# Performance work log

Hardware: AMD Instinct MI355X
Metric: run time of the kernel (lower is better)

Reference implementation:

```python
import jax, jax.numpy as jnp
import numpy as np

EMB = 128
HID = 128
N = 1024


def setup_inputs() -> dict:
    key = jax.random.key(0)
    ks = jax.random.split(key, 10)
    s1 = 1.0 / np.sqrt(2 * EMB)
    s2 = 1.0 / np.sqrt(HID)
    return {
        "z1": jax.random.normal(ks[0], (N, EMB), jnp.float32),
        "z2": jax.random.normal(ks[1], (N, EMB), jnp.float32),
        "W1": jax.random.uniform(ks[2], (HID, 2 * EMB), jnp.float32, -s1, s1),
        "b1": jax.random.uniform(ks[3], (HID,), jnp.float32, -s1, s1),
        "W2": jax.random.uniform(ks[4], (HID, HID), jnp.float32, -s2, s2),
        "b2": jax.random.uniform(ks[5], (HID,), jnp.float32, -s2, s2),
        "W3": jax.random.uniform(ks[6], (1, HID), jnp.float32, -s2, s2),
        "b3": jax.random.uniform(ks[7], (1,), jnp.float32, -s2, s2),
    }


def reference(z1, z2, W1, b1, W2, b2, W3, b3):
    # pairs[i, j] = concat(z1[j], z2[i]); first Linear split into two matmuls
    # so the [n, n, 2*emb] concat tensor is never materialized (same math).
    W1a = W1[:, :EMB]   # acts on z1 half
    W1b = W1[:, EMB:]   # acts on z2 half
    a = jnp.einsum('jd,hd->jh', z1, W1a)          # [n, h], varies along j
    b = jnp.einsum('id,hd->ih', z2, W1b)          # [n, h], varies along i
    h1 = jax.nn.gelu(a[None, :, :] + b[:, None, :] + b1, approximate=False)  # [n, n, h]
    h2 = jax.nn.gelu(jnp.einsum('ijh,gh->ijg', h1, W2) + b2, approximate=False)
    log_q = jnp.einsum('ijh,oh->ijo', h2, W3) + b3  # [n, n, 1]
    return log_q[..., 0]
```

## Files before the change

kernel.cpp:

```cpp
#include <hip/hip_runtime.h>

#define NN  1024
#define EMB 128
#define HID 128

typedef __attribute__((ext_vector_type(4))) float float4v;
typedef __attribute__((ext_vector_type(8))) float float8v;
typedef __attribute__((ext_vector_type(8))) short short8;
typedef __attribute__((ext_vector_type(4))) __bf16 bf16x4;
typedef __attribute__((ext_vector_type(8))) __bf16 bf16x8;

__device__ __forceinline__ short8 to_bf16x8(float4v a, float4v b) {
  float8v f = {a[0], a[1], a[2], a[3], b[0], b[1], b[2], b[3]};
  bf16x8 r = __builtin_convertvector(f, bf16x8);
  return __builtin_bit_cast(short8, r);
}

__device__ __forceinline__ void store_bf16x4(short* p, float4v v) {
  bf16x4 r = __builtin_convertvector(v, bf16x4);
  *(bf16x4*)p = r;
}

__device__ __forceinline__ float4v gelu4(float4v x) {
  float4v x2 = x * x;
  float4v t = x2 * 0.1029432f + 2.3022086f;
  float4v y = x * t;
  float4v e;
  e[0] = __builtin_amdgcn_exp2f(y[0]);
  e[1] = __builtin_amdgcn_exp2f(y[1]);
  e[2] = __builtin_amdgcn_exp2f(y[2]);
  e[3] = __builtin_amdgcn_exp2f(y[3]);
  float4v d = e + 1.0f;
  float p01 = d[0] * d[1];
  float p23 = d[2] * d[3];
  float rall = __builtin_amdgcn_rcpf(p01 * p23);
  float r01 = p23 * rall;
  float r23 = p01 * rall;
  float4v rv;
  rv[0] = d[1] * r01;
  rv[1] = d[0] * r01;
  rv[2] = d[3] * r23;
  rv[3] = d[2] * r23;
  return x - x * rv;
}

__device__ __forceinline__ float4v mfma16(short8 a, short8 b, float4v c) {
  return __builtin_amdgcn_mfma_f32_16x16x32_bf16(a, b, c, 0, 0, 0);
}

__global__ __launch_bounds__(256)
void prep_kernel(const float* __restrict__ z1, const float* __restrict__ z2,
                 const float* __restrict__ W1, const float* __restrict__ b1,
                 const float* __restrict__ W2,
                 float* __restrict__ Abuf, float* __restrict__ Bbuf,
                 unsigned short* __restrict__ W2f) {
  int blk = blockIdx.x, tid = threadIdx.x;
  if (blk < 128) {
    int which = blk >> 6;
    int j0 = (blk & 63) << 4;
    const float* z = which ? z2 : z1;
    __shared__ __align__(16) short zf[4 * 64 * 8];
    __shared__ __align__(16) short w1f[HID * HID];

    {
      int row = tid >> 4;
      int col = (tid & 15) * 8;
      const float* zp = z + (j0 + row) * EMB + col;
      float4v v0 = *(const float4v*)zp;
      float4v v1 = *(const float4v*)(zp + 4);
      int kt = col >> 5;
      int lane = ((col >> 3) & 3) * 16 + row;
      *(short8*)(zf + (kt * 64 + lane) * 8) = to_bf16x8(v0, v1);
    }
    {
      const float* wbase = W1 + which * EMB;
#pragma unroll
      for (int p = 0; p < 16; ++p) {
        int u = p * 256 + tid;
        int g = u >> 5;
        int c = (u & 31) * 4;
        float4v v = *(const float4v*)(wbase + g * (2 * EMB) + c);
        int kt = c >> 5;
        int nt = g >> 4;
        int lane = ((c >> 3) & 3) * 16 + (g & 15);
        store_bf16x4(w1f + ((kt * 8 + nt) * 64 + lane) * 8 + (c & 7), v);
      }
    }
    __syncthreads();

    int w = tid >> 6, l = tid & 63, r = l & 15, q = l >> 4;
    float4v acc0 = {}, acc1 = {};
#pragma unroll
    for (int kt = 0; kt < 4; ++kt) {
      short8 az  = *(const short8*)(zf + (kt * 64 + l) * 8);
      short8 bf0 = *(const short8*)(w1f + ((kt * 8 + w * 2) * 64 + l) * 8);
      short8 bf1 = *(const short8*)(w1f + ((kt * 8 + w * 2 + 1) * 64 + l) * 8);
      acc0 = mfma16(az, bf0, acc0);
      acc1 = mfma16(az, bf1, acc1);
    }
    float ba0 = which ? 0.0f : b1[w * 32 + r];
    float ba1 = which ? 0.0f : b1[w * 32 + 16 + r];
    float* dstp = which ? Bbuf : Abuf;
#pragma unroll
    for (int reg = 0; reg < 4; ++reg) {
      int row = j0 + q * 4 + reg;
      dstp[row * HID + w * 32 + r]      = acc0[reg] + ba0;
      dstp[row * HID + w * 32 + 16 + r] = acc1[reg] + ba1;
    }
  } else {
    int idx = (blk - 128) * 2048 + tid * 8;
    int lane = (idx >> 3) & 63;
    int nt = (idx >> 9) & 7;
    int kt = idx >> 12;
    int g = nt * 16 + (lane & 15);
    int hb = kt * 32 + (lane >> 4) * 8;
#pragma unroll
    for (int j = 0; j < 8; ++j) {
      unsigned u = __float_as_uint(W2[g * HID + hb + j]);
      W2f[idx + j] = (unsigned short)((u + 0x7FFFu + ((u >> 16) & 1u)) >> 16);
    }
  }
}

__global__ __launch_bounds__(512, 6)
void fused_mlp_kernel(const float* __restrict__ Abuf, const float* __restrict__ Bbuf,
                      const float* __restrict__ W2f4,
                      const float* __restrict__ b2, const float* __restrict__ W3,
                      const float* __restrict__ b3, float* __restrict__ out) {
  __shared__ __align__(16) short s_w2[HID * HID];

  int tid = threadIdx.x;
  {
    const float4v* src = (const float4v*)W2f4;
    float4v* dst = (float4v*)s_w2;
#pragma unroll
    for (int t = 0; t < 4; ++t)
      dst[tid + t * 512] = src[tid + t * 512];
  }

  int w = tid >> 6, l = tid & 63, r = l & 15, q = l >> 4;
  int bi = (blockIdx.x >> 6) << 3;
  int bj = (blockIdx.x & 63) << 4;

  const float* Arow = Abuf + (bj + r) * HID;
  const float* Brow = Bbuf + (bi + w) * HID;

  float4v acc[8];
#pragma unroll
  for (int nt = 0; nt < 8; ++nt) {
    float bv = b2[nt * 16 + r];
    acc[nt] = (float4v){bv, bv, bv, bv};
  }

  __syncthreads();

#pragma unroll
  for (int kt = 0; kt < 4; ++kt) {
    int h0 = kt * 32 + q * 8;
    float4v a0 = *(const float4v*)(Arow + h0);
    float4v a1 = *(const float4v*)(Arow + h0 + 4);
    float4v c0 = *(const float4v*)(Brow + h0);
    float4v c1 = *(const float4v*)(Brow + h0 + 4);
    short8 af = to_bf16x8(gelu4(a0 + c0), gelu4(a1 + c1));

    const short8* wrow = (const short8*)s_w2 + kt * 8 * 64 + l;
#pragma unroll
    for (int nt = 0; nt < 8; ++nt)
      acc[nt] = mfma16(af, wrow[nt * 64], acc[nt]);
  }

  float4v s = {0.f, 0.f, 0.f, 0.f};
#pragma unroll
  for (int nt = 0; nt < 8; ++nt) {
    float wv = W3[nt * 16 + r];
    s = s + gelu4(acc[nt]) * wv;
  }
#pragma unroll
  for (int mask = 1; mask < 16; mask <<= 1) {
#pragma unroll
    for (int reg = 0; reg < 4; ++reg)
      s[reg] += __shfl_xor(s[reg], mask, 64);
  }
  if (r < 4) {
    int irow = bi + w;
    int jcol = bj + q * 4 + r;
    out[irow * NN + jcol] = s[r] + b3[0];
  }
}

extern "C" void kernel_launch(void* const* d_in, const int* in_sizes, int n_in,
                              void* d_out, int out_size, void* d_ws, size_t ws_size,
                              hipStream_t stream) {
  const float* z1 = (const float*)d_in[0];
  const float* z2 = (const float*)d_in[1];
  const float* W1 = (const float*)d_in[2];
  const float* b1 = (const float*)d_in[3];
  const float* W2 = (const float*)d_in[4];
  const float* b2 = (const float*)d_in[5];
  const float* W3 = (const float*)d_in[6];
  const float* b3 = (const float*)d_in[7];
  float* out = (float*)d_out;

  float* Abuf = (float*)d_ws;
  float* Bbuf = Abuf + NN * HID;
  unsigned short* W2f = (unsigned short*)(Bbuf + NN * HID);

  prep_kernel<<<136, 256, 0, stream>>>(z1, z2, W1, b1, W2, Abuf, Bbuf, W2f);
  fused_mlp_kernel<<<(NN / 8) * (NN / 16), 512, 0, stream>>>(
      Abuf, Bbuf, (const float*)W2f, b2, W3, b3, out);
}
```

Before: 168.3 us.

## Give each wave two i-rows, swap MFMA operands, and split prep across more blocks

The fused kernel now uses 256 threads per block, and each wave computes two i-rows. Each LDS W2 fragment load therefore feeds two MFMAs, halving LDS traffic per output, and the W2 fragment is passed as the A operand so the output lands with hidden units along registers. The epilogue then uses vector W3/b2 loads and needs only two cross-lane shuffles instead of a 16-lane butterfly. The prep kernel splits the W1 projection across twice as many blocks and makes the W2 reads coalesced. The cost is more accumulator registers per thread (16 float4 accumulators), which may lower occupancy.

After: 158.1 us. 6.0% less time.

```diff
diff --git a/kernel.cpp b/kernel.cpp
--- a/kernel.cpp
+++ b/kernel.cpp
@@ -55,74 +55,75 @@
                  float* __restrict__ Abuf, float* __restrict__ Bbuf,
                  unsigned short* __restrict__ W2f) {
   int blk = blockIdx.x, tid = threadIdx.x;
-  if (blk < 128) {
-    int which = blk >> 6;
-    int j0 = (blk & 63) << 4;
+  if (blk < 256) {
+    int which = blk >> 7;
+    int j0 = ((blk & 127) >> 1) << 4;
+    int hh = blk & 1;
     const float* z = which ? z2 : z1;
     __shared__ __align__(16) short zf[4 * 64 * 8];
-    __shared__ __align__(16) short w1f[HID * HID];
-
+    __shared__ __align__(16) short w1f[16 * 64 * 8];
+
+#pragma unroll
+    for (int p = 0; p < 2; ++p) {
+      int u = p * 256 + tid;
+      int row = u >> 5;
+      int c = (u & 31) * 4;
+      float4v v = *(const float4v*)(z + (j0 + row) * EMB + c);
+      int kt = c >> 5;
+      int lane = ((c >> 3) & 3) * 16 + row;
+      store_bf16x4(zf + (kt * 64 + lane) * 8 + (c & 7), v);
+    }
     {
-      int row = tid >> 4;
-      int col = (tid & 15) * 8;
-      const float* zp = z + (j0 + row) * EMB + col;
-      float4v v0 = *(const float4v*)zp;
-      float4v v1 = *(const float4v*)(zp + 4);
-      int kt = col >> 5;
-      int lane = ((col >> 3) & 3) * 16 + row;
-      *(short8*)(zf + (kt * 64 + lane) * 8) = to_bf16x8(v0, v1);
-    }
-    {
-      const float* wbase = W1 + which * EMB;
-#pragma unroll
-      for (int p = 0; p < 16; ++p) {
+      const float* wbase = W1 + (hh * 64) * (2 * EMB) + which * EMB;
+#pragma unroll
+      for (int p = 0; p < 8; ++p) {
         int u = p * 256 + tid;
-        int g = u >> 5;
+        int grow = u >> 5;
         int c = (u & 31) * 4;
-        float4v v = *(const float4v*)(wbase + g * (2 * EMB) + c);
+        float4v v = *(const float4v*)(wbase + grow * (2 * EMB) + c);
         int kt = c >> 5;
-        int nt = g >> 4;
-        int lane = ((c >> 3) & 3) * 16 + (g & 15);
-        store_bf16x4(w1f + ((kt * 8 + nt) * 64 + lane) * 8 + (c & 7), v);
+        int ntl = grow >> 4;
+        int lane = ((c >> 3) & 3) * 16 + (grow & 15);
+        store_bf16x4(w1f + ((kt * 4 + ntl) * 64 + lane) * 8 + (c & 7), v);
       }
     }
     __syncthreads();
 
     int w = tid >> 6, l = tid & 63, r = l & 15, q = l >> 4;
-    float4v acc0 = {}, acc1 = {};
+    float4v acc = {};
 #pragma unroll
     for (int kt = 0; kt < 4; ++kt) {
-      short8 az  = *(const short8*)(zf + (kt * 64 + l) * 8);
-      short8 bf0 = *(const short8*)(w1f + ((kt * 8 + w * 2) * 64 + l) * 8);
-      short8 bf1 = *(const short8*)(w1f + ((kt * 8 + w * 2 + 1) * 64 + l) * 8);
-      acc0 = mfma16(az, bf0, acc0);
-      acc1 = mfma16(az, bf1, acc1);
-    }
-    float ba0 = which ? 0.0f : b1[w * 32 + r];
-    float ba1 = which ? 0.0f : b1[w * 32 + 16 + r];
+      short8 az = *(const short8*)(zf + (kt * 64 + l) * 8);
+      short8 bf = *(const short8*)(w1f + ((kt * 4 + w) * 64 + l) * 8);
+      acc = mfma16(az, bf, acc);
+    }
+    int gg = hh * 64 + w * 16 + r;
+    float ba = which ? 0.0f : b1[gg];
     float* dstp = which ? Bbuf : Abuf;
 #pragma unroll
-    for (int reg = 0; reg < 4; ++reg) {
-      int row = j0 + q * 4 + reg;
-      dstp[row * HID + w * 32 + r]      = acc0[reg] + ba0;
-      dstp[row * HID + w * 32 + 16 + r] = acc1[reg] + ba1;
-    }
+    for (int reg = 0; reg < 4; ++reg)
+      dstp[(j0 + q * 4 + reg) * HID + gg] = acc[reg] + ba;
   } else {
-    int idx = (blk - 128) * 2048 + tid * 8;
-    int lane = (idx >> 3) & 63;
-    int nt = (idx >> 9) & 7;
-    int kt = idx >> 12;
-    int g = nt * 16 + (lane & 15);
-    int hb = kt * 32 + (lane >> 4) * 8;
+    int s0 = (blk - 256) * 2048 + tid * 8;
+    float4v v0 = *(const float4v*)(W2 + s0);
+    float4v v1 = *(const float4v*)(W2 + s0 + 4);
+    float vals[8] = {v0[0], v0[1], v0[2], v0[3], v1[0], v1[1], v1[2], v1[3]};
 #pragma unroll
     for (int j = 0; j < 8; ++j) {
-      unsigned u = __float_as_uint(W2[g * HID + hb + j]);
-      W2f[idx + j] = (unsigned short)((u + 0x7FFFu + ((u >> 16) & 1u)) >> 16);
-    }
-  }
-}
-
-__global__ __launch_bounds__(512, 6)
+      int s = s0 + j;
+      int g = s >> 7;
+      int h = s & 127;
+      int kt = h >> 5;
+      int nt = g >> 4;
+      int lane = ((h >> 3) & 3) * 16 + (g & 15);
+      int dst = ((kt * 8 + nt) * 64 + lane) * 8 + (h & 7);
+      unsigned u = __float_as_uint(vals[j]);
+      W2f[dst] = (unsigned short)((u + 0x7FFFu + ((u >> 16) & 1u)) >> 16);
+    }
+  }
+}
+
+__global__ __launch_bounds__(256, 4)
 void fused_mlp_kernel(const float* __restrict__ Abuf, const float* __restrict__ Bbuf,
                       const float* __restrict__ W2f4,
                       const float* __restrict__ b2, const float* __restrict__ W3,
@@ -134,8 +135,8 @@
     const float4v* src = (const float4v*)W2f4;
     float4v* dst = (float4v*)s_w2;
 #pragma unroll
-    for (int t = 0; t < 4; ++t)
-      dst[tid + t * 512] = src[tid + t * 512];
+    for (int t = 0; t < 8; ++t)
+      dst[tid + t * 256] = src[tid + t * 256];
   }
 
   int w = tid >> 6, l = tid & 63, r = l & 15, q = l >> 4;
@@ -143,13 +144,15 @@
   int bj = (blockIdx.x & 63) << 4;
 
   const float* Arow = Abuf + (bj + r) * HID;
-  const float* Brow = Bbuf + (bi + w) * HID;
-
-  float4v acc[8];
+  const float* B0 = Bbuf + (bi + 2 * w) * HID;
+  const float* B1 = B0 + HID;
+
+  float4v acc[2][8];
 #pragma unroll
   for (int nt = 0; nt < 8; ++nt) {
-    float bv = b2[nt * 16 + r];
-    acc[nt] = (float4v){bv, bv, bv, bv};
+    float4v bv = *(const float4v*)(b2 + nt * 16 + q * 4);
+    acc[0][nt] = bv;
+    acc[1][nt] = bv;
   }
 
   __syncthreads();
@@ -159,32 +162,35 @@
     int h0 = kt * 32 + q * 8;
     float4v a0 = *(const float4v*)(Arow + h0);
     float4v a1 = *(const float4v*)(Arow + h0 + 4);
-    float4v c0 = *(const float4v*)(Brow + h0);
-    float4v c1 = *(const float4v*)(Brow + h0 + 4);
-    short8 af = to_bf16x8(gelu4(a0 + c0), gelu4(a1 + c1));
+
+    short8 af0 = to_bf16x8(gelu4(a0 + *(const float4v*)(B0 + h0)),
+                           gelu4(a1 + *(const float4v*)(B0 + h0 + 4)));
+    short8 af1 = to_bf16x8(gelu4(a0 + *(const float4v*)(B1 + h0)),
+                           gelu4(a1 + *(const float4v*)(B1 + h0 + 4)));
 
     const short8* wrow = (const short8*)s_w2 + kt * 8 * 64 + l;
 #pragma unroll
-    for (int nt = 0; nt < 8; ++nt)
-      acc[nt] = mfma16(af, wrow[nt * 64], acc[nt]);
-  }
-
-  float4v s = {0.f, 0.f, 0.f, 0.f};
-#pragma unroll
-  for (int nt = 0; nt < 8; ++nt) {
-    float wv = W3[nt * 16 + r];
-    s = s + gelu4(acc[nt]) * wv;
-  }
-#pragma unroll
-  for (int mask = 1; mask < 16; mask <<= 1) {
-#pragma unroll
-    for (int reg = 0; reg < 4; ++reg)
-      s[reg] += __shfl_xor(s[reg], mask, 64);
-  }
-  if (r < 4) {
-    int irow = bi + w;
-    int jcol = bj + q * 4 + r;
-    out[irow * NN + jcol] = s[r] + b3[0];
+    for (int nt = 0; nt < 8; ++nt) {
+      short8 wf = wrow[nt * 64];
+      acc[0][nt] = mfma16(wf, af0, acc[0][nt]);
+      acc[1][nt] = mfma16(wf, af1, acc[1][nt]);
+    }
+  }
+
+  float bias3 = b3[0];
+#pragma unroll
+  for (int p = 0; p < 2; ++p) {
+    float4v s = {0.f, 0.f, 0.f, 0.f};
+#pragma unroll
+    for (int nt = 0; nt < 8; ++nt) {
+      float4v wv = *(const float4v*)(W3 + nt * 16 + q * 4);
+      s = s + gelu4(acc[p][nt]) * wv;
+    }
+    float sc = s[0] + s[1] + s[2] + s[3];
+    sc += __shfl_xor(sc, 16, 64);
+    sc += __shfl_xor(sc, 32, 64);
+    if (l < 16)
+      out[(bi + 2 * w + p) * NN + bj + l] = sc + bias3;
   }
 }
 
@@ -205,7 +211,7 @@
   float* Bbuf = Abuf + NN * HID;
   unsigned short* W2f = (unsigned short*)(Bbuf + NN * HID);
 
-  prep_kernel<<<136, 256, 0, stream>>>(z1, z2, W1, b1, W2, Abuf, Bbuf, W2f);
-  fused_mlp_kernel<<<(NN / 8) * (NN / 16), 512, 0, stream>>>(
+  prep_kernel<<<264, 256, 0, stream>>>(z1, z2, W1, b1, W2, Abuf, Bbuf, W2f);
+  fused_mlp_kernel<<<(NN / 8) * (NN / 16), 256, 0, stream>>>(
       Abuf, Bbuf, (const float*)W2f, b2, W3, b3, out);
 }
```
